# Performance work log

Measured on AMD Instinct MI355X. Metric: run time of the kernel, lower is better.

The kernel has to match this reference:

```python
import jax, jax.numpy as jnp
import numpy as np

B, T, D_OBS = 64, 512, 128
D_LAT, D_HID, K = 16, 256, 8
VAR = 0.0005
LOG2PI = float(np.log(2.0 * np.pi))


def _leaky(x):
    return jnp.where(x > 0, x, 0.01 * x)


def setup_inputs() -> dict:
    key = jax.random.key(0)
    ks = jax.random.split(key, 12)
    s = 0.05
    return {
        "x": jax.random.normal(ks[0], (B, T, D_OBS), jnp.float32),
        "eps": jax.random.normal(ks[1], (B, T, D_LAT), jnp.float32),
        "W1": jax.random.normal(ks[2], (D_OBS, D_HID), jnp.float32) * s,
        "b1": jnp.zeros((D_HID,), jnp.float32),
        "W2": jax.random.normal(ks[3], (D_HID, 2 * D_LAT), jnp.float32) * s,
        "b2": jnp.zeros((2 * D_LAT,), jnp.float32),
        "Wt1": jax.random.normal(ks[4], (K, D_LAT, D_HID), jnp.float32) * s,
        "bt1": jnp.zeros((K, D_HID), jnp.float32),
        "Wt2": jax.random.normal(ks[5], (K, D_HID, D_LAT), jnp.float32) * s,
        "bt2": jnp.zeros((K, D_LAT), jnp.float32),
        "Wd1": jax.random.normal(ks[6], (D_LAT, D_HID), jnp.float32) * s,
        "bd1": jnp.zeros((D_HID,), jnp.float32),
        "Wd2": jax.random.normal(ks[7], (D_HID, D_OBS), jnp.float32) * s,
        "bd2": jnp.zeros((D_OBS,), jnp.float32),
        "Q": jax.random.normal(ks[8], (K, K), jnp.float32) * 0.1,
        "pi": jax.random.normal(ks[9], (K,), jnp.float32) * 0.1,
        "init_mean": jax.random.normal(ks[10], (K, D_LAT), jnp.float32),
        "init_cov": jax.random.uniform(ks[11], (K, 1, 1), jnp.float32) * jnp.eye(D_LAT, dtype=jnp.float32)[None] * 5.0,
        "covs": jnp.tile(jnp.eye(D_LAT, dtype=jnp.float32)[None], (K, 1, 1)),
    }


def _mvn_logprob(diff, chol):
    # diff [..., K, d]; chol [K, d, d] lower Cholesky of per-state covariance
    d = chol.shape[-1]
    Linv = jax.scipy.linalg.solve_triangular(
        chol, jnp.broadcast_to(jnp.eye(d, dtype=chol.dtype), chol.shape), lower=True)
    sol = jnp.einsum('kij,...kj->...ki', Linv, diff)
    logdet = 2.0 * jnp.sum(jnp.log(jnp.diagonal(chol, axis1=-2, axis2=-1)), -1)  # [K]
    return -0.5 * (d * LOG2PI + logdet + jnp.sum(sol * sol, -1))


def _forward(x, eps, W1, b1, W2, b2, Wt1, bt1, Wt2, bt2, Wd1, bd1, Wd2, bd2,
             Q, pi, init_mean, init_cov, covs):
    Bx = x.shape[0]
    dz = init_mean.shape[-1]
    # ---- factored MLP encoder: x -> (mu, logvar); reparameterized sample ----
    h = _leaky(x @ W1 + b1)
    enc = h @ W2 + b2
    z_mu, z_log_var = enc[..., :dz], enc[..., dz:]
    z = z_mu + jnp.exp(0.5 * z_log_var) * eps                            # [B,T,dz]
    # ---- local evidence log p(z_t | z_{t-1}, s_t=k) ----
    jitter = 1e-6 * jnp.eye(dz, dtype=x.dtype)
    L0 = jnp.linalg.cholesky(init_cov @ jnp.swapaxes(init_cov, -1, -2) + jitter)
    ev1 = _mvn_logprob(z[:, 0:1, None, :] - init_mean[None, None], L0)   # [B,1,K]
    ht = jax.nn.softplus(jnp.einsum('btd,kdh->btkh', z[:, :-1], Wt1) + bt1)
    means = jnp.einsum('btkh,khd->btkd', ht, Wt2) + bt2                  # [B,T-1,K,dz]
    Lt = jnp.linalg.cholesky(covs @ jnp.swapaxes(covs, -1, -2) + jitter)
    evT = _mvn_logprob(z[:, 1:, None, :] - means, Lt)                    # [B,T-1,K]
    ev = jnp.concatenate([ev1, evT], axis=1)                             # [B,T,K]
    # ---- HMM alpha recursion in log domain (temperature=1) ----
    log_pi = jax.nn.log_softmax(pi)
    Qlog = jax.nn.log_softmax(Q, axis=-1).T                              # [new, old]
    lp0 = ev[:, 0] + log_pi
    lZ0 = jax.scipy.special.logsumexp(lp0, axis=-1)
    la0 = lp0 - lZ0[:, None]

    def step(la, ev_t):
        lp = jax.scipy.special.logsumexp(ev_t[:, :, None] + Qlog[None] + la[:, None, :], axis=-1)
        lZ = jax.scipy.special.logsumexp(lp, axis=-1)
        return lp - lZ[:, None], lZ

    _, lZs = jax.lax.scan(step, la0, jnp.moveaxis(ev[:, 1:], 1, 0))
    log_Z = lZ0 + jnp.sum(lZs, axis=0)                                   # [B]
    # ---- decoder ----
    x_hat = _leaky(z @ Wd1 + bd1) @ Wd2 + bd2
    # ---- ELBO ----
    recon = jnp.sum(-0.5 * jnp.log(2.0 * jnp.pi * VAR) - (x - x_hat) ** 2 / (2.0 * VAR)) / Bx
    logq = -0.5 * (dz * LOG2PI + jnp.sum(z_log_var, -1)
                   + jnp.sum((z - z_mu) ** 2 / jnp.exp(z_log_var), -1))
    entropy_q = -jnp.sum(logq) / Bx
    msm = jnp.sum(log_Z) / Bx
    loss = -(recon + entropy_q + msm)
    return x_hat, z, loss


def reference(x, eps, W1, b1, W2, b2, Wt1, bt1, Wt2, bt2, Wd1, bd1, Wd2, bd2,
              Q, pi, init_mean, init_cov, covs):
    return _forward(x, eps, W1, b1, W2, b2, Wt1, bt1, Wt2, bt2, Wd1, bd1, Wd2, bd2,
                    Q, pi, init_mean, init_cov, covs)
```

## Files before the change

kernel.cpp:

```cpp
#include <hip/hip_runtime.h>
#include <math.h>

#define B_SZ   64
#define T_SZ   512
#define DOBS   128
#define DLAT   16
#define DHID   256
#define K_SZ   8
#define ROWS_A 32768

#define LOG2PI_F 1.8378770664093453f
#define VAR_F    5.0e-4f

#define LINV0_OFF   16
#define LOGDET0_OFF 2064
#define LINVT_OFF   2080
#define LOGDETT_OFF 4128
#define WIMG_F_OFF  8192

#define EVT_W1   0
#define EVT_W2   49152
#define EVT_LINV 82944
#define ENC_W1   86016
#define ENC_W2   120832
#define DEC_W1   129280
#define DEC_W2   135424
#define WCVT_TOTAL 141568

#define Z_OUT_OFF   4194304
#define LOSS_OFF    4718592
#define PBUF_OFF  262144
#define ACC_OFF   327680

typedef __attribute__((ext_vector_type(8))) short short8;
typedef __attribute__((ext_vector_type(8))) unsigned short ush8;
typedef __attribute__((ext_vector_type(4))) float floatx4;

__device__ __forceinline__ float leakyf(float v) { return v > 0.f ? v : 0.01f * v; }
__device__ __forceinline__ unsigned short f2bf(float f) {
  union { float f; unsigned int u; } v; v.f = f;
  unsigned int lsb = (v.u >> 16) & 1;
  v.u += 0x7fffu + lsb;
  return (unsigned short)(v.u >> 16);
}

__global__ __launch_bounds__(256) void prep_kernel(const float* __restrict__ init_cov,
                                                   const float* __restrict__ covs,
                                                   float* __restrict__ ws) {
  __shared__ float M[16][16];
  __shared__ float L[16][16];
  __shared__ float X[16][17];
  int job = blockIdx.x;
  const float* C = (job < 8) ? (init_cov + job * 256) : (covs + (job - 8) * 256);
  float* linv = ws + ((job < 8) ? (LINV0_OFF + job * 256) : (LINVT_OFF + (job - 8) * 256));
  float* logdet = ws + ((job < 8) ? (LOGDET0_OFF + job) : (LOGDETT_OFF + (job - 8)));
  int tid = threadIdx.x;
  if (job == 0 && tid < 4) ws[tid] = 0.f;
  int i = tid >> 4, j = tid & 15;
  {
    float s = (i == j) ? 1e-6f : 0.f;
    #pragma unroll
    for (int p = 0; p < 16; ++p) s += C[i * 16 + p] * C[j * 16 + p];
    M[i][j] = s;
  }
  __syncthreads();
  for (int c = 0; c < 16; ++c) {
    if (tid == 0) {
      float s = M[c][c];
      for (int p = 0; p < c; ++p) s -= L[c][p] * L[c][p];
      L[c][c] = sqrtf(s);
    }
    __syncthreads();
    if (tid > c && tid < 16) {
      float s = M[tid][c];
      for (int p = 0; p < c; ++p) s -= L[tid][p] * L[c][p];
      L[tid][c] = s / L[c][c];
    }
    __syncthreads();
  }
  if (tid < 16) {
    for (int r = 0; r < 16; ++r) {
      float s = (r == tid) ? 1.f : 0.f;
      for (int p = tid; p < r; ++p) s -= L[r][p] * X[p][tid];
      X[r][tid] = (r >= tid) ? s / L[r][r] : 0.f;
    }
  }
  __syncthreads();
  linv[i * 16 + j] = X[i][j];
  if (tid == 0) {
    float s = 0.f;
    for (int d = 0; d < 16; ++d) s += logf(L[d][d]);
    *logdet = 2.f * s;
  }
}

__global__ __launch_bounds__(256) void wcvt_kernel(
    const float* __restrict__ Wt1, const float* __restrict__ Wt2,
    const float* __restrict__ W1, const float* __restrict__ W2,
    const float* __restrict__ Wd1, const float* __restrict__ Wd2,
    const float* __restrict__ ws, unsigned short* __restrict__ wimg) {
  for (int e = blockIdx.x * 256 + threadIdx.x; e < WCVT_TOTAL; e += gridDim.x * 256) {
    if (e < 32768) {
      int k = e >> 12, r = e & 4095, i = r >> 4, d = r & 15;
      wimg[EVT_W1 + k * 6144 + i * 24 + d] = f2bf(Wt1[k * 4096 + d * 256 + i]);
    } else if (e < 65536) {
      int e2 = e - 32768; int k = e2 >> 12, r = e2 & 4095, h = r >> 4, d2 = r & 15;
      wimg[EVT_W2 + k * 4224 + d2 * 264 + h] = f2bf(Wt2[k * 4096 + h * 16 + d2]);
    } else if (e < 67584) {
      int e2 = e - 65536; int k = e2 >> 8, r = e2 & 255, i = r >> 4, j = r & 15;
      wimg[EVT_LINV + k * 384 + i * 24 + j] = f2bf(ws[LINVT_OFF + k * 256 + i * 16 + j]);
    } else if (e < 100352) {
      int e2 = e - 67584; int n = e2 >> 7, kk = e2 & 127;
      wimg[ENC_W1 + n * 136 + kk] = f2bf(W1[kk * 256 + n]);
    } else if (e < 108544) {
      int e2 = e - 100352; int n = e2 >> 8, kk = e2 & 255;
      wimg[ENC_W2 + n * 264 + kk] = f2bf(W2[kk * 32 + n]);
    } else if (e < 112640) {
      int e2 = e - 108544; int n = e2 >> 4, kk = e2 & 15;
      wimg[DEC_W1 + n * 24 + kk] = f2bf(Wd1[kk * 256 + n]);
    } else {
      int e2 = e - 112640; int n = e2 & 127, kk = e2 >> 7;
      wimg[DEC_W2 + n * 264 + kk] = f2bf(Wd2[kk * 128 + n]);
    }
  }
}

__global__ __launch_bounds__(256) void enc_kernel(
    const float* __restrict__ x, const float* __restrict__ eps,
    const float* __restrict__ b1, const float* __restrict__ b2,
    const unsigned short* __restrict__ wimg,
    float* __restrict__ z_out, float* __restrict__ ws) {
  __shared__ __align__(16) unsigned short w2t[32 * 264];
  __shared__ __align__(16) unsigned short ttile[4][16 * 56];
  __shared__ float b1s[256];
  __shared__ float sred;
  int tid = threadIdx.x;
  if (tid == 0) sred = 0.f;
  {
    const ush8* s2 = (const ush8*)(wimg + ENC_W2);
    for (int e = tid; e < 1056; e += 256) ((ush8*)w2t)[e] = s2[e];
    b1s[tid] = b1[tid];
  }
  __syncthreads();

  int wid = tid >> 6, lane = tid & 63;
  int m = lane & 15, quad = lane >> 4;
  unsigned short* tt = ttile[wid];
  const unsigned short* w1i = wimg + ENC_W1;
  long rowb = (long)blockIdx.x * 64 + wid * 16;

  short8 xa[4];
  const float* xp = x + (rowb + m) * 128 + quad * 8;
  #pragma unroll
  for (int kt = 0; kt < 4; ++kt) {
    float4 f0 = *(const float4*)(xp + kt * 32);
    float4 f1 = *(const float4*)(xp + kt * 32 + 4);
    short8 v;
    v[0] = (short)f2bf(f0.x); v[1] = (short)f2bf(f0.y);
    v[2] = (short)f2bf(f0.z); v[3] = (short)f2bf(f0.w);
    v[4] = (short)f2bf(f1.x); v[5] = (short)f2bf(f1.y);
    v[6] = (short)f2bf(f1.z); v[7] = (short)f2bf(f1.w);
    xa[kt] = v;
  }
  float bm0 = b2[m], bm1 = b2[16 + m];
  floatx4 a20 = {bm0, bm0, bm0, bm0};
  floatx4 a21 = {bm1, bm1, bm1, bm1};
  #pragma unroll
  for (int cp = 0; cp < 8; ++cp) {
    #pragma unroll
    for (int h = 0; h < 2; ++h) {
      int c = cp * 2 + h;
      float bias = b1s[c * 16 + m];
      floatx4 a1 = {bias, bias, bias, bias};
      #pragma unroll
      for (int kt = 0; kt < 4; ++kt) {
        short8 bf = *(const short8*)&w1i[(c * 16 + m) * 136 + kt * 32 + quad * 8];
        a1 = __builtin_amdgcn_mfma_f32_16x16x32_bf16(xa[kt], bf, a1, 0, 0, 0);
      }
      #pragma unroll
      for (int g = 0; g < 4; ++g)
        tt[(quad * 4 + g) * 56 + h * 16 + m] = f2bf(leakyf(a1[g]));
    }
    short8 ha = *(const short8*)&tt[m * 56 + quad * 8];
    short8 wb0 = *(const short8*)&w2t[m * 264 + cp * 32 + quad * 8];
    short8 wb1 = *(const short8*)&w2t[(16 + m) * 264 + cp * 32 + quad * 8];
    a20 = __builtin_amdgcn_mfma_f32_16x16x32_bf16(ha, wb0, a20, 0, 0, 0);
    a21 = __builtin_amdgcn_mfma_f32_16x16x32_bf16(ha, wb1, a21, 0, 0, 0);
  }
  float logq_acc = 0.f;
  #pragma unroll
  for (int g = 0; g < 4; ++g) {
    long row = rowb + quad * 4 + g;
    float mu = a20[g], lv = a21[g];
    float ev = eps[row * 16 + m];
    float zv = mu + __expf(0.5f * lv) * ev;
    z_out[row * 16 + m] = zv;
    float zz = zv - mu;
    logq_acc += lv + zz * zz * __expf(-lv);
  }
  #pragma unroll
  for (int off = 1; off < 64; off <<= 1) logq_acc += __shfl_xor(logq_acc, off, 64);
  if (lane == 0) atomicAdd(&sred, -0.5f * logq_acc);
  __syncthreads();
  if (tid == 0) atomicAdd(&ws[1], sred - 0.5f * 16.f * LOG2PI_F * 64.f);
}

__global__ __launch_bounds__(256) void evt_kernel(
    const float* __restrict__ z, const unsigned short* __restrict__ wimg,
    const float* __restrict__ bt1, const float* __restrict__ bt2,
    const float* __restrict__ ws, float* __restrict__ evT) {
  __shared__ __align__(16) unsigned short w1t[6144];
  __shared__ __align__(16) unsigned short w2t[4224];
  __shared__ __align__(16) unsigned short linvb[384];
  __shared__ __align__(16) unsigned short ttile[4][16 * 56];
  __shared__ __align__(16) unsigned short dtile[4][16 * 24];
  __shared__ float bt1s[256];
  int tid = threadIdx.x;
  int k = blockIdx.y;
  {
    const ush8* s1 = (const ush8*)(wimg + EVT_W1 + k * 6144);
    for (int e = tid; e < 768; e += 256) ((ush8*)w1t)[e] = s1[e];
    const ush8* s2 = (const ush8*)(wimg + EVT_W2 + k * 4224);
    for (int e = tid; e < 528; e += 256) ((ush8*)w2t)[e] = s2[e];
    if (tid < 48) ((ush8*)linvb)[tid] = ((const ush8*)(wimg + EVT_LINV + k * 384))[tid];
    bt1s[tid] = bt1[k * 256 + tid];
  }
  float logdetk = ws[LOGDETT_OFF + k];
  __syncthreads();

  int wid = tid >> 6, lane = tid & 63;
  int m = lane & 15, quad = lane >> 4;
  unsigned short* tt = ttile[wid];
  unsigned short* db = dtile[wid];
  float btv = bt2[k * 16 + m];

  #pragma unroll
  for (int tile = 0; tile < 4; ++tile) {
    long rowb = (long)blockIdx.x * 256 + wid * 64 + tile * 16;
    short8 za = (short8)0;
    if (quad < 2) {
      const float* zp = z + (rowb + m) * 16 + quad * 8;
      float4 f0 = *(const float4*)zp;
      float4 f1 = *(const float4*)(zp + 4);
      za[0] = (short)f2bf(f0.x); za[1] = (short)f2bf(f0.y);
      za[2] = (short)f2bf(f0.z); za[3] = (short)f2bf(f0.w);
      za[4] = (short)f2bf(f1.x); za[5] = (short)f2bf(f1.y);
      za[6] = (short)f2bf(f1.z); za[7] = (short)f2bf(f1.w);
    }
    floatx4 a2 = {btv, btv, btv, btv};
    #pragma unroll
    for (int cp = 0; cp < 8; ++cp) {
      #pragma unroll
      for (int h = 0; h < 2; ++h) {
        int c = cp * 2 + h;
        short8 bfrag = (short8)0;
        if (quad < 2) bfrag = *(const short8*)&w1t[(c * 16 + m) * 24 + quad * 8];
        float bias = bt1s[c * 16 + m];
        floatx4 a1 = {bias, bias, bias, bias};
        a1 = __builtin_amdgcn_mfma_f32_16x16x32_bf16(za, bfrag, a1, 0, 0, 0);
        #pragma unroll
        for (int g = 0; g < 4; ++g) {
          float v = a1[g];
          float t = __expf(-fabsf(v));
          float sp = fmaxf(v, 0.f) + __logf(1.f + t);
          tt[(quad * 4 + g) * 56 + h * 16 + m] = f2bf(sp);
        }
      }
      short8 ha = *(const short8*)&tt[m * 56 + quad * 8];
      short8 wb = *(const short8*)&w2t[m * 264 + cp * 32 + quad * 8];
      a2 = __builtin_amdgcn_mfma_f32_16x16x32_bf16(ha, wb, a2, 0, 0, 0);
    }
    #pragma unroll
    for (int g = 0; g < 4; ++g) {
      long grow = rowb + quad * 4 + g;
      float znx = (grow + 1 < ROWS_A) ? z[(grow + 1) * 16 + m] : 0.f;
      db[(quad * 4 + g) * 24 + m] = f2bf(znx - a2[g]);
    }
    short8 da = (short8)0, lb = (short8)0;
    if (quad < 2) {
      da = *(const short8*)&db[m * 24 + quad * 8];
      lb = *(const short8*)&linvb[m * 24 + quad * 8];
    }
    floatx4 a3 = {0.f, 0.f, 0.f, 0.f};
    a3 = __builtin_amdgcn_mfma_f32_16x16x32_bf16(da, lb, a3, 0, 0, 0);
    #pragma unroll
    for (int g = 0; g < 4; ++g) {
      float v = a3[g];
      v = v * v;
      v += __shfl_xor(v, 1, 64);
      v += __shfl_xor(v, 2, 64);
      v += __shfl_xor(v, 4, 64);
      v += __shfl_xor(v, 8, 64);
      long grow = rowb + quad * 4 + g;
      if (m == 0 && (grow & 511) != 511) {
        long r1 = grow + 1;
        evT[(r1 >> 9) * 4096 + (long)k * 512 + (r1 & 511)] =
            -0.5f * (16.f * LOG2PI_F + logdetk + v);
      }
    }
  }
}

__global__ __launch_bounds__(256) void hmm_scan(const float* __restrict__ Q,
                                                const float* __restrict__ evT,
                                                float* __restrict__ pbuf,
                                                float* __restrict__ accbuf) {
  int tid = threadIdx.x;
  int wid = tid >> 6, lane = tid & 63;
  int job = blockIdx.x * 4 + wid;
  int b = job >> 4, c = job & 15;
  int i = lane >> 3, j = lane & 7;

  float qp[8];
  #pragma unroll
  for (int p = 0; p < 8; ++p) {
    float mr = Q[p * 8 + 0];
    #pragma unroll
    for (int cc = 1; cc < 8; ++cc) mr = fmaxf(mr, Q[p * 8 + cc]);
    float rs = 0.f;
    #pragma unroll
    for (int cc = 0; cc < 8; ++cc) rs += __expf(Q[p * 8 + cc] - mr);
    qp[p] = __expf(Q[p * 8 + i] - mr) / rs;
  }
  float qself;
  {
    float mr = Q[j * 8 + 0];
    #pragma unroll
    for (int cc = 1; cc < 8; ++cc) mr = fmaxf(mr, Q[j * 8 + cc]);
    float rs = 0.f;
    #pragma unroll
    for (int cc = 0; cc < 8; ++cc) rs += __expf(Q[j * 8 + cc] - mr);
    qself = __expf(Q[j * 8 + i] - mr) / rs;
  }

  int t0 = 1 + c * 32;
  int L = (c == 15) ? 31 : 32;
  const float* evI = evT + (long)b * 4096 + (long)i * 512 + t0;

  float f[32];
  float accm = 0.f;
  #pragma unroll
  for (int s = 0; s < 32; ++s) {
    float e = (s < L) ? evI[s] : 0.f;
    float m = e;
    m = fmaxf(m, __shfl_xor(m, 8, 64));
    m = fmaxf(m, __shfl_xor(m, 16, 64));
    m = fmaxf(m, __shfl_xor(m, 32, 64));
    f[s] = __expf(e - m);
    if (s < L) accm += m;
  }

  float P = f[0] * qself;
  #pragma unroll
  for (int s = 1; s < 32; ++s) {
    if (s < L) {
      float a0 = __shfl(P, j,      64);
      float a1 = __shfl(P, 8 + j,  64);
      float a2 = __shfl(P, 16 + j, 64);
      float a3 = __shfl(P, 24 + j, 64);
      float a4 = __shfl(P, 32 + j, 64);
      float a5 = __shfl(P, 40 + j, 64);
      float a6 = __shfl(P, 48 + j, 64);
      float a7 = __shfl(P, 56 + j, 64);
      float sv = ((qp[0] * a0 + qp[1] * a1) + (qp[2] * a2 + qp[3] * a3))
               + ((qp[4] * a4 + qp[5] * a5) + (qp[6] * a6 + qp[7] * a7));
      P = f[s] * sv;
    }
    if ((s & 7) == 7) {
      float mx = P;
      mx = fmaxf(mx, __shfl_xor(mx, 1, 64));
      mx = fmaxf(mx, __shfl_xor(mx, 2, 64));
      mx = fmaxf(mx, __shfl_xor(mx, 4, 64));
      mx = fmaxf(mx, __shfl_xor(mx, 8, 64));
      mx = fmaxf(mx, __shfl_xor(mx, 16, 64));
      mx = fmaxf(mx, __shfl_xor(mx, 32, 64));
      mx = fmaxf(mx, 1e-30f);
      P = P / mx;
      accm += __logf(mx);
    }
  }
  pbuf[(long)job * 64 + lane] = P;
  if (lane == 0) accbuf[job] = accm;
}

__global__ __launch_bounds__(512) void hmm_comb(const float* __restrict__ pi,
                                                const float* __restrict__ z,
                                                const float* __restrict__ init_mean,
                                                const float* __restrict__ pbuf,
                                                const float* __restrict__ accbuf,
                                                float* __restrict__ ws) {
  int tid = threadIdx.x;
  int wid = tid >> 6, lane = tid & 63;
  int b = blockIdx.x * 8 + wid;
  int j = lane & 7;

  float mp = pi[0];
  #pragma unroll
  for (int cc = 1; cc < 8; ++cc) mp = fmaxf(mp, pi[cc]);
  float sp = 0.f;
  #pragma unroll
  for (int cc = 0; cc < 8; ++cc) sp += __expf(pi[cc] - mp);
  float lpi = pi[j] - mp - __logf(sp);

  const float* zr = z + (long)b * 8192;
  const float* linv = ws + LINV0_OFF + j * 256;
  float diff[16];
  #pragma unroll
  for (int d = 0; d < 16; ++d) diff[d] = zr[d] - init_mean[j * 16 + d];
  float quad0 = 0.f;
  #pragma unroll
  for (int i2 = 0; i2 < 16; ++i2) {
    float s = 0.f;
    #pragma unroll
    for (int jj = 0; jj < 16; ++jj) s += linv[i2 * 16 + jj] * diff[jj];
    quad0 += s * s;
  }
  float ev0 = -0.5f * (16.f * LOG2PI_F + ws[LOGDET0_OFF + j] + quad0);

  float lp0 = ev0 + lpi;
  float m0 = lp0;
  m0 = fmaxf(m0, __shfl_xor(m0, 1, 64));
  m0 = fmaxf(m0, __shfl_xor(m0, 2, 64));
  m0 = fmaxf(m0, __shfl_xor(m0, 4, 64));
  float u = __expf(lp0 - m0);
  double acc = (double)m0;

  #pragma unroll
  for (int c = 0; c < 16; ++c) {
    float P = pbuf[((long)b * 16 + c) * 64 + lane];
    float contrib = P * u;
    contrib += __shfl_xor(contrib, 1, 64);
    contrib += __shfl_xor(contrib, 2, 64);
    contrib += __shfl_xor(contrib, 4, 64);
    u = __shfl(contrib, j * 9, 64);
    float mxu = u;
    mxu = fmaxf(mxu, __shfl_xor(mxu, 1, 64));
    mxu = fmaxf(mxu, __shfl_xor(mxu, 2, 64));
    mxu = fmaxf(mxu, __shfl_xor(mxu, 4, 64));
    mxu = fmaxf(mxu, 1e-30f);
    u = u / mxu;
    acc += (double)(__logf(mxu) + accbuf[b * 16 + c]);
  }
  float su = u;
  su += __shfl_xor(su, 1, 64);
  su += __shfl_xor(su, 2, 64);
  su += __shfl_xor(su, 4, 64);
  float logZ = (float)(acc + (double)__logf(su));
  if (lane == 0) atomicAdd(&ws[2], logZ);
}

__global__ __launch_bounds__(256) void dec_kernel(
    const float* __restrict__ x, const float* __restrict__ z,
    const float* __restrict__ bd1, const float* __restrict__ bd2,
    const unsigned short* __restrict__ wimg,
    float* __restrict__ xhat, float* __restrict__ ws) {
  __shared__ __align__(16) unsigned short w1t[6144];
  __shared__ __align__(16) unsigned short ttile[4][16 * 56];
  __shared__ float bd1s[256];
  __shared__ float bd2s[128];
  __shared__ float sred;
  int tid = threadIdx.x;
  if (tid == 0) sred = 0.f;
  {
    const ush8* s1 = (const ush8*)(wimg + DEC_W1);
    for (int e = tid; e < 768; e += 256) ((ush8*)w1t)[e] = s1[e];
    bd1s[tid] = bd1[tid];
    if (tid < 128) bd2s[tid] = bd2[tid];
  }
  __syncthreads();

  int wid = tid >> 6, lane = tid & 63;
  int m = lane & 15, quad = lane >> 4;
  unsigned short* tt = ttile[wid];
  const unsigned short* w2i = wimg + DEC_W2;
  long rowb = (long)blockIdx.x * 64 + wid * 16;

  short8 za = (short8)0;
  if (quad < 2) {
    const float* zp = z + (rowb + m) * 16 + quad * 8;
    float4 f0 = *(const float4*)zp;
    float4 f1 = *(const float4*)(zp + 4);
    za[0] = (short)f2bf(f0.x); za[1] = (short)f2bf(f0.y);
    za[2] = (short)f2bf(f0.z); za[3] = (short)f2bf(f0.w);
    za[4] = (short)f2bf(f1.x); za[5] = (short)f2bf(f1.y);
    za[6] = (short)f2bf(f1.z); za[7] = (short)f2bf(f1.w);
  }
  floatx4 a2[8];
  #pragma unroll
  for (int c2 = 0; c2 < 8; ++c2) {
    float bv = bd2s[c2 * 16 + m];
    a2[c2] = (floatx4){bv, bv, bv, bv};
  }
  #pragma unroll
  for (int cp = 0; cp < 8; ++cp) {
    #pragma unroll
    for (int h = 0; h < 2; ++h) {
      int c = cp * 2 + h;
      short8 bfrag = (short8)0;
      if (quad < 2) bfrag = *(const short8*)&w1t[(c * 16 + m) * 24 + quad * 8];
      float bias = bd1s[c * 16 + m];
      floatx4 a1 = {bias, bias, bias, bias};
      a1 = __builtin_amdgcn_mfma_f32_16x16x32_bf16(za, bfrag, a1, 0, 0, 0);
      #pragma unroll
      for (int g = 0; g < 4; ++g)
        tt[(quad * 4 + g) * 56 + h * 16 + m] = f2bf(leakyf(a1[g]));
    }
    short8 ha = *(const short8*)&tt[m * 56 + quad * 8];
    #pragma unroll
    for (int c2 = 0; c2 < 8; ++c2) {
      short8 wb = *(const short8*)&w2i[(c2 * 16 + m) * 264 + cp * 32 + quad * 8];
      a2[c2] = __builtin_amdgcn_mfma_f32_16x16x32_bf16(ha, wb, a2[c2], 0, 0, 0);
    }
  }
  const float C0 = -0.5f * logf(6.2831853071795864f * VAR_F);
  float rsum = 0.f;
  #pragma unroll
  for (int c2 = 0; c2 < 8; ++c2) {
    int col = c2 * 16 + m;
    #pragma unroll
    for (int g = 0; g < 4; ++g) {
      long row = rowb + quad * 4 + g;
      float xh = a2[c2][g];
      xhat[row * 128 + col] = xh;
      float dd = x[row * 128 + col] - xh;
      rsum += C0 - dd * dd * (0.5f / VAR_F);
    }
  }
  #pragma unroll
  for (int off = 1; off < 64; off <<= 1) rsum += __shfl_xor(rsum, off, 64);
  if (lane == 0) atomicAdd(&sred, rsum);
  __syncthreads();
  if (tid == 0) atomicAdd(&ws[0], sred);
}

__global__ void fin_kernel(const float* __restrict__ ws, float* __restrict__ out) {
  float loss = -((ws[0] - ws[1] + ws[2]) * (1.f / 64.f));
  out[LOSS_OFF] = loss;
}

extern "C" void kernel_launch(void* const* d_in, const int* in_sizes, int n_in,
                              void* d_out, int out_size, void* d_ws, size_t ws_size,
                              hipStream_t stream) {
  (void)in_sizes; (void)n_in; (void)out_size; (void)ws_size;
  const float* x   = (const float*)d_in[0];
  const float* eps = (const float*)d_in[1];
  const float* W1  = (const float*)d_in[2];
  const float* b1  = (const float*)d_in[3];
  const float* W2  = (const float*)d_in[4];
  const float* b2  = (const float*)d_in[5];
  const float* Wt1 = (const float*)d_in[6];
  const float* bt1 = (const float*)d_in[7];
  const float* Wt2 = (const float*)d_in[8];
  const float* bt2 = (const float*)d_in[9];
  const float* Wd1 = (const float*)d_in[10];
  const float* bd1 = (const float*)d_in[11];
  const float* Wd2 = (const float*)d_in[12];
  const float* bd2 = (const float*)d_in[13];
  const float* Q   = (const float*)d_in[14];
  const float* pi  = (const float*)d_in[15];
  const float* im  = (const float*)d_in[16];
  const float* ic  = (const float*)d_in[17];
  const float* cv  = (const float*)d_in[18];
  float* out = (float*)d_out;
  float* ws  = (float*)d_ws;
  float* z_out = out + Z_OUT_OFF;
  float* evT  = out;
  float* pbuf = out + PBUF_OFF;
  float* accb = out + ACC_OFF;
  unsigned short* wimg = (unsigned short*)(ws + WIMG_F_OFF);

  prep_kernel<<<16, 256, 0, stream>>>(ic, cv, ws);
  wcvt_kernel<<<144, 256, 0, stream>>>(Wt1, Wt2, W1, W2, Wd1, Wd2, ws, wimg);
  enc_kernel<<<512, 256, 0, stream>>>(x, eps, b1, b2, wimg, z_out, ws);
  evt_kernel<<<dim3(128, 8), 256, 0, stream>>>(z_out, wimg, bt1, bt2, ws, evT);
  hmm_scan<<<256, 256, 0, stream>>>(Q, evT, pbuf, accb);
  hmm_comb<<<8, 512, 0, stream>>>(pi, z_out, im, pbuf, accb, ws);
  dec_kernel<<<512, 256, 0, stream>>>(x, z_out, bd1, bd2, wimg, out, ws);
  fin_kernel<<<1, 1, 0, stream>>>(ws, out);
}
```

Measured before the change: 252.2 us.

## Read weights from global/L2 directly, quadruple evt grid, use double atomics for reductions

Removes the shared-memory staging of weights and biases in the encoder, transition-evidence and decoder kernels. B fragments are now read straight from global memory (expected to hit in L2/cache), and biases are kept in registers, which drops the block-wide syncs and cuts LDS usage. The evt kernel goes from four row tiles per wave to one, with the grid quadrupled to keep full coverage. This should raise parallelism and occupancy. Per-block shared reductions become per-wave double-precision global atomics, which improves accumulation precision but adds more atomic traffic and redundant weight fetches.

```diff
diff --git a/kernel.cpp b/kernel.cpp
--- a/kernel.cpp
+++ b/kernel.cpp
@@ -55,7 +55,7 @@
   float* linv = ws + ((job < 8) ? (LINV0_OFF + job * 256) : (LINVT_OFF + (job - 8) * 256));
   float* logdet = ws + ((job < 8) ? (LOGDET0_OFF + job) : (LOGDETT_OFF + (job - 8)));
   int tid = threadIdx.x;
-  if (job == 0 && tid < 4) ws[tid] = 0.f;
+  if (job == 0 && tid < 8) ws[tid] = 0.f;
   int i = tid >> 4, j = tid & 15;
   {
     float s = (i == j) ? 1e-6f : 0.f;
@@ -130,24 +130,18 @@
     const float* __restrict__ b1, const float* __restrict__ b2,
     const unsigned short* __restrict__ wimg,
     float* __restrict__ z_out, float* __restrict__ ws) {
-  __shared__ __align__(16) unsigned short w2t[32 * 264];
   __shared__ __align__(16) unsigned short ttile[4][16 * 56];
-  __shared__ float b1s[256];
-  __shared__ float sred;
   int tid = threadIdx.x;
-  if (tid == 0) sred = 0.f;
-  {
-    const ush8* s2 = (const ush8*)(wimg + ENC_W2);
-    for (int e = tid; e < 1056; e += 256) ((ush8*)w2t)[e] = s2[e];
-    b1s[tid] = b1[tid];
-  }
-  __syncthreads();
-
   int wid = tid >> 6, lane = tid & 63;
   int m = lane & 15, quad = lane >> 4;
   unsigned short* tt = ttile[wid];
   const unsigned short* w1i = wimg + ENC_W1;
+  const unsigned short* w2i = wimg + ENC_W2;
   long rowb = (long)blockIdx.x * 64 + wid * 16;
+
+  float b1r[16];
+  #pragma unroll
+  for (int c = 0; c < 16; ++c) b1r[c] = b1[c * 16 + m];
 
   short8 xa[4];
   const float* xp = x + (rowb + m) * 128 + quad * 8;
@@ -170,7 +164,7 @@
     #pragma unroll
     for (int h = 0; h < 2; ++h) {
       int c = cp * 2 + h;
-      float bias = b1s[c * 16 + m];
+      float bias = b1r[c];
       floatx4 a1 = {bias, bias, bias, bias};
       #pragma unroll
       for (int kt = 0; kt < 4; ++kt) {
@@ -182,8 +176,8 @@
         tt[(quad * 4 + g) * 56 + h * 16 + m] = f2bf(leakyf(a1[g]));
     }
     short8 ha = *(const short8*)&tt[m * 56 + quad * 8];
-    short8 wb0 = *(const short8*)&w2t[m * 264 + cp * 32 + quad * 8];
-    short8 wb1 = *(const short8*)&w2t[(16 + m) * 264 + cp * 32 + quad * 8];
+    short8 wb0 = *(const short8*)&w2i[m * 264 + cp * 32 + quad * 8];
+    short8 wb1 = *(const short8*)&w2i[(16 + m) * 264 + cp * 32 + quad * 8];
     a20 = __builtin_amdgcn_mfma_f32_16x16x32_bf16(ha, wb0, a20, 0, 0, 0);
     a21 = __builtin_amdgcn_mfma_f32_16x16x32_bf16(ha, wb1, a21, 0, 0, 0);
   }
@@ -200,103 +194,92 @@
   }
   #pragma unroll
   for (int off = 1; off < 64; off <<= 1) logq_acc += __shfl_xor(logq_acc, off, 64);
-  if (lane == 0) atomicAdd(&sred, -0.5f * logq_acc);
-  __syncthreads();
-  if (tid == 0) atomicAdd(&ws[1], sred - 0.5f * 16.f * LOG2PI_F * 64.f);
+  if (lane == 0) {
+    double v = -0.5 * ((double)logq_acc + 16.0 * 16.0 * (double)LOG2PI_F);
+    atomicAdd((double*)ws + 1, v);
+  }
 }
 
 __global__ __launch_bounds__(256) void evt_kernel(
     const float* __restrict__ z, const unsigned short* __restrict__ wimg,
     const float* __restrict__ bt1, const float* __restrict__ bt2,
     const float* __restrict__ ws, float* __restrict__ evT) {
-  __shared__ __align__(16) unsigned short w1t[6144];
-  __shared__ __align__(16) unsigned short w2t[4224];
-  __shared__ __align__(16) unsigned short linvb[384];
   __shared__ __align__(16) unsigned short ttile[4][16 * 56];
   __shared__ __align__(16) unsigned short dtile[4][16 * 24];
-  __shared__ float bt1s[256];
   int tid = threadIdx.x;
   int k = blockIdx.y;
-  {
-    const ush8* s1 = (const ush8*)(wimg + EVT_W1 + k * 6144);
-    for (int e = tid; e < 768; e += 256) ((ush8*)w1t)[e] = s1[e];
-    const ush8* s2 = (const ush8*)(wimg + EVT_W2 + k * 4224);
-    for (int e = tid; e < 528; e += 256) ((ush8*)w2t)[e] = s2[e];
-    if (tid < 48) ((ush8*)linvb)[tid] = ((const ush8*)(wimg + EVT_LINV + k * 384))[tid];
-    bt1s[tid] = bt1[k * 256 + tid];
-  }
-  float logdetk = ws[LOGDETT_OFF + k];
-  __syncthreads();
-
   int wid = tid >> 6, lane = tid & 63;
   int m = lane & 15, quad = lane >> 4;
   unsigned short* tt = ttile[wid];
   unsigned short* db = dtile[wid];
+  const unsigned short* w1i = wimg + EVT_W1 + k * 6144;
+  const unsigned short* w2i = wimg + EVT_W2 + k * 4224;
+  const unsigned short* li  = wimg + EVT_LINV + k * 384;
+  float logdetk = ws[LOGDETT_OFF + k];
   float btv = bt2[k * 16 + m];
-
-  #pragma unroll
-  for (int tile = 0; tile < 4; ++tile) {
-    long rowb = (long)blockIdx.x * 256 + wid * 64 + tile * 16;
-    short8 za = (short8)0;
-    if (quad < 2) {
-      const float* zp = z + (rowb + m) * 16 + quad * 8;
-      float4 f0 = *(const float4*)zp;
-      float4 f1 = *(const float4*)(zp + 4);
-      za[0] = (short)f2bf(f0.x); za[1] = (short)f2bf(f0.y);
-      za[2] = (short)f2bf(f0.z); za[3] = (short)f2bf(f0.w);
-      za[4] = (short)f2bf(f1.x); za[5] = (short)f2bf(f1.y);
-      za[6] = (short)f2bf(f1.z); za[7] = (short)f2bf(f1.w);
-    }
-    floatx4 a2 = {btv, btv, btv, btv};
-    #pragma unroll
-    for (int cp = 0; cp < 8; ++cp) {
+  float bt1r[16];
+  #pragma unroll
+  for (int c = 0; c < 16; ++c) bt1r[c] = bt1[k * 256 + c * 16 + m];
+  short8 lb = (short8)0;
+  if (quad < 2) lb = *(const short8*)&li[m * 24 + quad * 8];
+
+  long rowb = (long)blockIdx.x * 64 + wid * 16;
+  short8 za = (short8)0;
+  if (quad < 2) {
+    const float* zp = z + (rowb + m) * 16 + quad * 8;
+    float4 f0 = *(const float4*)zp;
+    float4 f1 = *(const float4*)(zp + 4);
+    za[0] = (short)f2bf(f0.x); za[1] = (short)f2bf(f0.y);
+    za[2] = (short)f2bf(f0.z); za[3] = (short)f2bf(f0.w);
+    za[4] = (short)f2bf(f1.x); za[5] = (short)f2bf(f1.y);
+    za[6] = (short)f2bf(f1.z); za[7] = (short)f2bf(f1.w);
+  }
+  floatx4 a2 = {btv, btv, btv, btv};
+  #pragma unroll
+  for (int cp = 0; cp < 8; ++cp) {
+    #pragma unroll
+    for (int h = 0; h < 2; ++h) {
+      int c = cp * 2 + h;
+      short8 bfrag = (short8)0;
+      if (quad < 2) bfrag = *(const short8*)&w1i[(c * 16 + m) * 24 + quad * 8];
+      float bias = bt1r[c];
+      floatx4 a1 = {bias, bias, bias, bias};
+      a1 = __builtin_amdgcn_mfma_f32_16x16x32_bf16(za, bfrag, a1, 0, 0, 0);
       #pragma unroll
-      for (int h = 0; h < 2; ++h) {
-        int c = cp * 2 + h;
-        short8 bfrag = (short8)0;
-        if (quad < 2) bfrag = *(const short8*)&w1t[(c * 16 + m) * 24 + quad * 8];
-        float bias = bt1s[c * 16 + m];
-        floatx4 a1 = {bias, bias, bias, bias};
-        a1 = __builtin_amdgcn_mfma_f32_16x16x32_bf16(za, bfrag, a1, 0, 0, 0);
-        #pragma unroll
-        for (int g = 0; g < 4; ++g) {
-          float v = a1[g];
-          float t = __expf(-fabsf(v));
-          float sp = fmaxf(v, 0.f) + __logf(1.f + t);
-          tt[(quad * 4 + g) * 56 + h * 16 + m] = f2bf(sp);
-        }
+      for (int g = 0; g < 4; ++g) {
+        float v = a1[g];
+        float t = __expf(-fabsf(v));
+        float sp = fmaxf(v, 0.f) + __logf(1.f + t);
+        tt[(quad * 4 + g) * 56 + h * 16 + m] = f2bf(sp);
       }
-      short8 ha = *(const short8*)&tt[m * 56 + quad * 8];
-      short8 wb = *(const short8*)&w2t[m * 264 + cp * 32 + quad * 8];
-      a2 = __builtin_amdgcn_mfma_f32_16x16x32_bf16(ha, wb, a2, 0, 0, 0);
-    }
-    #pragma unroll
-    for (int g = 0; g < 4; ++g) {
-      long grow = rowb + quad * 4 + g;
-      float znx = (grow + 1 < ROWS_A) ? z[(grow + 1) * 16 + m] : 0.f;
-      db[(quad * 4 + g) * 24 + m] = f2bf(znx - a2[g]);
-    }
-    short8 da = (short8)0, lb = (short8)0;
-    if (quad < 2) {
-      da = *(const short8*)&db[m * 24 + quad * 8];
-      lb = *(const short8*)&linvb[m * 24 + quad * 8];
-    }
-    floatx4 a3 = {0.f, 0.f, 0.f, 0.f};
-    a3 = __builtin_amdgcn_mfma_f32_16x16x32_bf16(da, lb, a3, 0, 0, 0);
-    #pragma unroll
-    for (int g = 0; g < 4; ++g) {
-      float v = a3[g];
-      v = v * v;
-      v += __shfl_xor(v, 1, 64);
-      v += __shfl_xor(v, 2, 64);
-      v += __shfl_xor(v, 4, 64);
-      v += __shfl_xor(v, 8, 64);
-      long grow = rowb + quad * 4 + g;
-      if (m == 0 && (grow & 511) != 511) {
-        long r1 = grow + 1;
-        evT[(r1 >> 9) * 4096 + (long)k * 512 + (r1 & 511)] =
-            -0.5f * (16.f * LOG2PI_F + logdetk + v);
-      }
+    }
+    short8 ha = *(const short8*)&tt[m * 56 + quad * 8];
+    short8 wb = *(const short8*)&w2i[m * 264 + cp * 32 + quad * 8];
+    a2 = __builtin_amdgcn_mfma_f32_16x16x32_bf16(ha, wb, a2, 0, 0, 0);
+  }
+  #pragma unroll
+  for (int g = 0; g < 4; ++g) {
+    long grow = rowb + quad * 4 + g;
+    float znx = (grow + 1 < ROWS_A) ? z[(grow + 1) * 16 + m] : 0.f;
+    db[(quad * 4 + g) * 24 + m] = f2bf(znx - a2[g]);
+  }
+  short8 da = (short8)0;
+  if (quad < 2) da = *(const short8*)&db[m * 24 + quad * 8];
+  floatx4 a3 = {0.f, 0.f, 0.f, 0.f};
+  a3 = __builtin_amdgcn_mfma_f32_16x16x32_bf16(da, lb, a3, 0, 0, 0);
+  #pragma unroll
+  for (int g = 0; g < 4; ++g) {
+    float v = a3[g];
+    v = v * v;
+    v += __shfl_xor(v, 1, 64);
+    v += __shfl_xor(v, 2, 64);
+    v += __shfl_xor(v, 4, 64);
+    v += __shfl_xor(v, 8, 64);
+    long grow = rowb + quad * 4 + g;
+    if (m == 0 && (grow & 511) != 511) {
+      long r1 = grow + 1;
+      evT[(r1 >> 9) * 4096 + (long)k * 512 + (r1 & 511)] =
+          -0.5f * (16.f * LOG2PI_F + logdetk + v);
     }
   }
 }
@@ -445,8 +428,8 @@
   su += __shfl_xor(su, 1, 64);
   su += __shfl_xor(su, 2, 64);
   su += __shfl_xor(su, 4, 64);
-  float logZ = (float)(acc + (double)__logf(su));
-  if (lane == 0) atomicAdd(&ws[2], logZ);
+  double logZ = acc + (double)__logf(su);
+  if (lane == 0) atomicAdd((double*)ws + 2, logZ);
 }
 
 __global__ __launch_bounds__(256) void dec_kernel(
@@ -454,26 +437,18 @@
     const float* __restrict__ bd1, const float* __restrict__ bd2,
     const unsigned short* __restrict__ wimg,
     float* __restrict__ xhat, float* __restrict__ ws) {
-  __shared__ __align__(16) unsigned short w1t[6144];
   __shared__ __align__(16) unsigned short ttile[4][16 * 56];
-  __shared__ float bd1s[256];
-  __shared__ float bd2s[128];
-  __shared__ float sred;
   int tid = threadIdx.x;
-  if (tid == 0) sred = 0.f;
-  {
-    const ush8* s1 = (const ush8*)(wimg + DEC_W1);
-    for (int e = tid; e < 768; e += 256) ((ush8*)w1t)[e] = s1[e];
-    bd1s[tid] = bd1[tid];
-    if (tid < 128) bd2s[tid] = bd2[tid];
-  }
-  __syncthreads();
-
   int wid = tid >> 6, lane = tid & 63;
   int m = lane & 15, quad = lane >> 4;
   unsigned short* tt = ttile[wid];
+  const unsigned short* w1i = wimg + DEC_W1;
   const unsigned short* w2i = wimg + DEC_W2;
   long rowb = (long)blockIdx.x * 64 + wid * 16;
+
+  float bd1r[16];
+  #pragma unroll
+  for (int c = 0; c < 16; ++c) bd1r[c] = bd1[c * 16 + m];
 
   short8 za = (short8)0;
   if (quad < 2) {
@@ -488,7 +463,7 @@
   floatx4 a2[8];
   #pragma unroll
   for (int c2 = 0; c2 < 8; ++c2) {
-    float bv = bd2s[c2 * 16 + m];
+    float bv = bd2[c2 * 16 + m];
     a2[c2] = (floatx4){bv, bv, bv, bv};
   }
   #pragma unroll
@@ -497,8 +472,8 @@
     for (int h = 0; h < 2; ++h) {
       int c = cp * 2 + h;
       short8 bfrag = (short8)0;
-      if (quad < 2) bfrag = *(const short8*)&w1t[(c * 16 + m) * 24 + quad * 8];
-      float bias = bd1s[c * 16 + m];
+      if (quad < 2) bfrag = *(const short8*)&w1i[(c * 16 + m) * 24 + quad * 8];
+      float bias = bd1r[c];
       floatx4 a1 = {bias, bias, bias, bias};
       a1 = __builtin_amdgcn_mfma_f32_16x16x32_bf16(za, bfrag, a1, 0, 0, 0);
       #pragma unroll
@@ -528,14 +503,13 @@
   }
   #pragma unroll
   for (int off = 1; off < 64; off <<= 1) rsum += __shfl_xor(rsum, off, 64);
-  if (lane == 0) atomicAdd(&sred, rsum);
-  __syncthreads();
-  if (tid == 0) atomicAdd(&ws[0], sred);
+  if (lane == 0) atomicAdd((double*)ws + 0, (double)rsum);
 }
 
 __global__ void fin_kernel(const float* __restrict__ ws, float* __restrict__ out) {
-  float loss = -((ws[0] - ws[1] + ws[2]) * (1.f / 64.f));
-  out[LOSS_OFF] = loss;
+  const double* dws = (const double*)ws;
+  double loss = -((dws[0] - dws[1] + dws[2]) * (1.0 / 64.0));
+  out[LOSS_OFF] = (float)loss;
 }
 
 extern "C" void kernel_launch(void* const* d_in, const int* in_sizes, int n_in,
@@ -572,7 +546,7 @@
   prep_kernel<<<16, 256, 0, stream>>>(ic, cv, ws);
   wcvt_kernel<<<144, 256, 0, stream>>>(Wt1, Wt2, W1, W2, Wd1, Wd2, ws, wimg);
   enc_kernel<<<512, 256, 0, stream>>>(x, eps, b1, b2, wimg, z_out, ws);
-  evt_kernel<<<dim3(128, 8), 256, 0, stream>>>(z_out, wimg, bt1, bt2, ws, evT);
+  evt_kernel<<<dim3(512, 8), 256, 0, stream>>>(z_out, wimg, bt1, bt2, ws, evT);
   hmm_scan<<<256, 256, 0, stream>>>(Q, evT, pbuf, accb);
   hmm_comb<<<8, 512, 0, stream>>>(pi, z_out, im, pbuf, accb, ws);
   dec_kernel<<<512, 256, 0, stream>>>(x, z_out, bd1, bd2, wimg, out, ws);
```

Result: slower. 281.1 us (+11.4%).
